# Kernel optimization log

Measured on AMD Instinct MI355X. Metric: run time of the kernel, lower is better.

The kernel has to match this reference:

```python
import jax, jax.numpy as jnp
import numpy as np

S, B, H, NL = 2048, 32, 1024, 2


def setup_inputs() -> dict:
    key = jax.random.key(0)
    k1, k2, k3, k4, k5 = jax.random.split(key, 5)
    hidden = jax.random.normal(k1, (NL, B, H), dtype=jnp.float32)
    encoder_outputs = jax.random.normal(k2, (S, B, H), dtype=jnp.float32)
    # nn.Linear(2H, H): weight [H, 2H], bias [H]
    attn_w = jax.random.normal(k3, (H, 2 * H), dtype=jnp.float32) / np.sqrt(2.0 * H)
    attn_b = jax.random.normal(k4, (H,), dtype=jnp.float32) * 0.01
    # v ~ N(0, 1/sqrt(H))
    v = jax.random.normal(k5, (H,), dtype=jnp.float32) / np.sqrt(H)
    return {"hidden": hidden, "encoder_outputs": encoder_outputs,
            "attn_w": attn_w, "attn_b": attn_b, "v": v}


def reference(hidden, encoder_outputs, attn_w, attn_b, v):
    # hidden: [NL, B, H]; encoder_outputs: [S, B, H]
    max_len = encoder_outputs.shape[0]
    h = jnp.broadcast_to(hidden[-1], (max_len,) + hidden[-1].shape)  # [S, B, H]
    x = jnp.concatenate([h, encoder_outputs], axis=2)                 # [S, B, 2H]
    energy = jnp.tanh(jnp.einsum('sbk,hk->sbh', x, attn_w) + attn_b)  # [S, B, H]
    scores = jnp.einsum('sbh,h->bs', energy, v)                       # [B, S]
    return jax.nn.softmax(scores, axis=1)
```

## Files before the change

### kernel.cpp

```cpp
#include <hip/hip_runtime.h>
#include <stdint.h>


#define S_LEN 2048
#define B_SZ 32
#define H_SZ 1024
#define M_TOT (S_LEN * B_SZ)
#define K_TOT H_SZ
#define NCB 8

typedef __attribute__((ext_vector_type(8))) short short8;
typedef __attribute__((ext_vector_type(4))) float f32x4;

static __device__ __forceinline__ unsigned short f2bf(float x) {
  uint32_t u = __builtin_bit_cast(uint32_t, x);
  u += 0x7FFFu + ((u >> 16) & 1u);
  return (unsigned short)(u >> 16);
}

static __device__ __forceinline__ float fast_tanh(float x) {
  float e = __expf(2.0f * x);
  return 1.0f - 2.0f / (e + 1.0f);
}

__global__ void __launch_bounds__(256) prep_u_kernel(
    const float* __restrict__ hidden, const float* __restrict__ attn_w,
    const float* __restrict__ attn_b, float* __restrict__ u) {
  __shared__ float hs[H_SZ];
  const int b = blockIdx.y, hc = blockIdx.x, tid = threadIdx.x;
  const float* hid = hidden + (size_t)1 * B_SZ * H_SZ + (size_t)b * H_SZ;
  for (int i = tid; i < H_SZ; i += 256) hs[i] = hid[i];
  __syncthreads();
  const int h = hc * 256 + tid;
  const float* wrow = attn_w + (size_t)h * (2 * H_SZ);
  float s = 0.f;
#pragma unroll 4
  for (int k = 0; k < H_SZ; k += 4) {
    float4 w4 = *reinterpret_cast<const float4*>(wrow + k);
    s += w4.x * hs[k] + w4.y * hs[k + 1] + w4.z * hs[k + 2] + w4.w * hs[k + 3];
  }
  u[(size_t)b * H_SZ + h] = s + attn_b[h];
}

__global__ void __launch_bounds__(256) prep_w2_kernel(
    const float* __restrict__ attn_w, unsigned short* __restrict__ Bt) {
  const int idx = blockIdx.x * 256 + threadIdx.x;
  const int base = idx * 4;
  const int n = base >> 10, k = base & 1023;
  float4 w = *reinterpret_cast<const float4*>(attn_w + (size_t)n * 2048 + 1024 + k);
  ushort4 o;
  o.x = f2bf(w.x); o.y = f2bf(w.y); o.z = f2bf(w.z); o.w = f2bf(w.w);
  *reinterpret_cast<ushort4*>(Bt + base) = o;
}

__global__ void __launch_bounds__(256) gemm_fused_kernel(
    const float* __restrict__ A,
    const unsigned short* __restrict__ Bt,
    const float* __restrict__ u,
    const float* __restrict__ v,
    float* __restrict__ pscore) {
  __shared__ unsigned short As[128 * 32];
  __shared__ unsigned short Bs[128 * 32];
  __shared__ float rowsum[2][128];

  const int tid = threadIdx.x;
  const int wid = tid >> 6, lane = tid & 63;
  const int wr = wid >> 1, wc = wid & 1;
  const int cb = blockIdx.x;
  const int brow = blockIdx.y * 128;
  const int bcol = cb * 128;

  const int arow_st = tid >> 1;
  const int acol_st = (tid & 1) * 16;
  const float* Ag = A + (size_t)(brow + arow_st) * K_TOT + acol_st;
  unsigned short* AsW = As + arow_st * 32 + acol_st;

  const int chunk0 = wid * 2;
  const unsigned short* Bg0 =
      Bt + (size_t)(bcol + chunk0 * 16 + (lane >> 2)) * K_TOT + (lane & 3) * 8;

  f32x4 acc[4][4];
#pragma unroll
  for (int i = 0; i < 4; ++i)
#pragma unroll
    for (int j = 0; j < 4; ++j) acc[i][j] = (f32x4){0.f, 0.f, 0.f, 0.f};

  const int fr = lane & 15;
  const int kseg = (lane >> 4) * 8;

  for (int k0 = 0; k0 < K_TOT; k0 += 32) {
    __syncthreads();
    const float4* ap = reinterpret_cast<const float4*>(Ag + k0);
    float4 f0 = ap[0], f1 = ap[1], f2 = ap[2], f3 = ap[3];
    uint4 w0, w1;
    w0.x = (uint32_t)f2bf(f0.x) | ((uint32_t)f2bf(f0.y) << 16);
    w0.y = (uint32_t)f2bf(f0.z) | ((uint32_t)f2bf(f0.w) << 16);
    w0.z = (uint32_t)f2bf(f1.x) | ((uint32_t)f2bf(f1.y) << 16);
    w0.w = (uint32_t)f2bf(f1.z) | ((uint32_t)f2bf(f1.w) << 16);
    w1.x = (uint32_t)f2bf(f2.x) | ((uint32_t)f2bf(f2.y) << 16);
    w1.y = (uint32_t)f2bf(f2.z) | ((uint32_t)f2bf(f2.w) << 16);
    w1.z = (uint32_t)f2bf(f3.x) | ((uint32_t)f2bf(f3.y) << 16);
    w1.w = (uint32_t)f2bf(f3.z) | ((uint32_t)f2bf(f3.w) << 16);
    *reinterpret_cast<uint4*>(AsW) = w0;
    *reinterpret_cast<uint4*>(AsW + 8) = w1;
    __builtin_amdgcn_global_load_lds(
        (const __attribute__((address_space(1))) void*)(Bg0 + k0),
        (__attribute__((address_space(3))) void*)(Bs + chunk0 * 512), 16, 0, 0);
    __builtin_amdgcn_global_load_lds(
        (const __attribute__((address_space(1))) void*)(Bg0 + 16 * K_TOT + k0),
        (__attribute__((address_space(3))) void*)(Bs + chunk0 * 512 + 512), 16, 0, 0);
    __syncthreads();

    short8 af[4], bf[4];
#pragma unroll
    for (int i = 0; i < 4; ++i)
      af[i] = *reinterpret_cast<const short8*>(As + (wr * 64 + i * 16 + fr) * 32 + kseg);
#pragma unroll
    for (int j = 0; j < 4; ++j)
      bf[j] = *reinterpret_cast<const short8*>(Bs + (wc * 64 + j * 16 + fr) * 32 + kseg);
#pragma unroll
    for (int i = 0; i < 4; ++i)
#pragma unroll
      for (int j = 0; j < 4; ++j)
        acc[i][j] = __builtin_amdgcn_mfma_f32_16x16x32_bf16(af[i], bf[j], acc[i][j], 0, 0, 0);
  }

  float vv[4];
#pragma unroll
  for (int j = 0; j < 4; ++j) vv[j] = v[bcol + wc * 64 + j * 16 + fr];

  const int g4 = (lane >> 4) * 4;
#pragma unroll
  for (int i = 0; i < 4; ++i) {
#pragma unroll
    for (int reg = 0; reg < 4; ++reg) {
      const int rloc = wr * 64 + i * 16 + g4 + reg;
      const int bb = (brow + rloc) & (B_SZ - 1);
      float rs = 0.f;
#pragma unroll
      for (int j = 0; j < 4; ++j) {
        const int h = bcol + wc * 64 + j * 16 + fr;
        float val = acc[i][j][reg] + u[(size_t)bb * H_SZ + h];
        rs += vv[j] * fast_tanh(val);
      }
      rs += __shfl_xor(rs, 1);
      rs += __shfl_xor(rs, 2);
      rs += __shfl_xor(rs, 4);
      rs += __shfl_xor(rs, 8);
      if (fr == 0) rowsum[wc][rloc] = rs;
    }
  }
  __syncthreads();
  if (tid < 128) {
    pscore[(size_t)cb * M_TOT + brow + tid] = rowsum[0][tid] + rowsum[1][tid];
  }
}

__global__ void __launch_bounds__(256) softmax_kernel(
    const float* __restrict__ ps, float* __restrict__ out) {
  const int b = blockIdx.x, tid = threadIdx.x;
  const int wid = tid >> 6, lane = tid & 63;
  __shared__ float sred[4];
  float vals[8];
  float mx = -1e30f;
#pragma unroll
  for (int ii = 0; ii < 8; ++ii) {
    const int s = ii * 256 + tid;
    float sum = 0.f;
#pragma unroll
    for (int cbk = 0; cbk < NCB; ++cbk) sum += ps[(size_t)cbk * M_TOT + s * B_SZ + b];
    vals[ii] = sum;
    mx = fmaxf(mx, sum);
  }
#pragma unroll
  for (int m = 1; m < 64; m <<= 1) mx = fmaxf(mx, __shfl_xor(mx, m));
  if (lane == 0) sred[wid] = mx;
  __syncthreads();
  mx = fmaxf(fmaxf(sred[0], sred[1]), fmaxf(sred[2], sred[3]));
  __syncthreads();
  float es = 0.f;
#pragma unroll
  for (int ii = 0; ii < 8; ++ii) {
    vals[ii] = __expf(vals[ii] - mx);
    es += vals[ii];
  }
#pragma unroll
  for (int m = 1; m < 64; m <<= 1) es += __shfl_xor(es, m);
  if (lane == 0) sred[wid] = es;
  __syncthreads();
  es = sred[0] + sred[1] + sred[2] + sred[3];
  const float inv = 1.0f / es;
#pragma unroll
  for (int ii = 0; ii < 8; ++ii) out[(size_t)b * S_LEN + ii * 256 + tid] = vals[ii] * inv;
}

extern "C" void kernel_launch(void* const* d_in, const int* in_sizes, int n_in,
                              void* d_out, int out_size, void* d_ws, size_t ws_size,
                              hipStream_t stream) {
  const float* hidden = (const float*)d_in[0];
  const float* enc    = (const float*)d_in[1];
  const float* attn_w = (const float*)d_in[2];
  const float* attn_b = (const float*)d_in[3];
  const float* v      = (const float*)d_in[4];
  float* out = (float*)d_out;

  char* w = (char*)d_ws;
  unsigned short* Bt = (unsigned short*)w;
  float* u  = (float*)(w + (size_t)2 * 1024 * 1024);
  float* ps = (float*)(w + (size_t)2 * 1024 * 1024 + 128 * 1024);

  prep_u_kernel<<<dim3(4, 32), 256, 0, stream>>>(hidden, attn_w, attn_b, u);
  prep_w2_kernel<<<1024, 256, 0, stream>>>(attn_w, Bt);
  gemm_fused_kernel<<<dim3(NCB, M_TOT / 128), 256, 0, stream>>>(enc, Bt, u, v, ps);
  softmax_kernel<<<B_SZ, 256, 0, stream>>>(ps, out);
}
```

Baseline: 406.1 us.

## Pre-convert encoder outputs to swizzled bf16 tile images and stream via LDS DMA

Measured after the change: 350.4 us. -13.7%, faster.

```diff
diff --git a/kernel.cpp b/kernel.cpp
--- a/kernel.cpp
+++ b/kernel.cpp
@@ -8,6 +8,8 @@
 #define M_TOT (S_LEN * B_SZ)
 #define K_TOT H_SZ
 #define NCB 8
+#define BK 64
+#define TILE_SHORTS 8192
 
 typedef __attribute__((ext_vector_type(8))) short short8;
 typedef __attribute__((ext_vector_type(4))) float f32x4;
@@ -17,7 +19,9 @@
   u += 0x7FFFu + ((u >> 16) & 1u);
   return (unsigned short)(u >> 16);
 }
-
+static __device__ __forceinline__ uint32_t pack2(float a, float b) {
+  return (uint32_t)f2bf(a) | ((uint32_t)f2bf(b) << 16);
+}
 static __device__ __forceinline__ float fast_tanh(float x) {
   float e = __expf(2.0f * x);
   return 1.0f - 2.0f / (e + 1.0f);
@@ -42,42 +46,60 @@
   u[(size_t)b * H_SZ + h] = s + attn_b[h];
 }
 
-__global__ void __launch_bounds__(256) prep_w2_kernel(
-    const float* __restrict__ attn_w, unsigned short* __restrict__ Bt) {
+__global__ void __launch_bounds__(256) prep_a_kernel(
+    const float* __restrict__ enc, unsigned short* __restrict__ Aimg) {
   const int idx = blockIdx.x * 256 + threadIdx.x;
-  const int base = idx * 4;
-  const int n = base >> 10, k = base & 1023;
-  float4 w = *reinterpret_cast<const float4*>(attn_w + (size_t)n * 2048 + 1024 + k);
-  ushort4 o;
-  o.x = f2bf(w.x); o.y = f2bf(w.y); o.z = f2bf(w.z); o.w = f2bf(w.w);
-  *reinterpret_cast<ushort4*>(Bt + base) = o;
-}
-
-__global__ void __launch_bounds__(256) gemm_fused_kernel(
-    const float* __restrict__ A,
-    const unsigned short* __restrict__ Bt,
-    const float* __restrict__ u,
-    const float* __restrict__ v,
+  const int m = idx >> 7, sl = idx & 127;
+  const int kb = sl >> 3, s8 = sl & 7;
+  const float4* src =
+      reinterpret_cast<const float4*>(enc + (size_t)m * K_TOT + kb * BK + s8 * 8);
+  float4 f0 = src[0], f1 = src[1];
+  uint4 o;
+  o.x = pack2(f0.x, f0.y); o.y = pack2(f0.z, f0.w);
+  o.z = pack2(f1.x, f1.y); o.w = pack2(f1.z, f1.w);
+  const int row = m & 127;
+  const size_t tile = (size_t)(m >> 7) * 16 + kb;
+  unsigned short* dst = Aimg + tile * TILE_SHORTS + row * 64 + ((s8 ^ (row & 7)) << 3);
+  *reinterpret_cast<uint4*>(dst) = o;
+}
+
+__global__ void __launch_bounds__(256) prep_b_kernel(
+    const float* __restrict__ attn_w, unsigned short* __restrict__ Bimg) {
+  const int idx = blockIdx.x * 256 + threadIdx.x;
+  const int n = idx >> 7, sl = idx & 127;
+  const int kb = sl >> 3, s8 = sl & 7;
+  const float4* src = reinterpret_cast<const float4*>(
+      attn_w + (size_t)n * 2048 + 1024 + kb * BK + s8 * 8);
+  float4 f0 = src[0], f1 = src[1];
+  uint4 o;
+  o.x = pack2(f0.x, f0.y); o.y = pack2(f0.z, f0.w);
+  o.z = pack2(f1.x, f1.y); o.w = pack2(f1.z, f1.w);
+  const int row = n & 127;
+  const size_t tile = (size_t)(n >> 7) * 16 + kb;
+  unsigned short* dst = Bimg + tile * TILE_SHORTS + row * 64 + ((s8 ^ (row & 7)) << 3);
+  *reinterpret_cast<uint4*>(dst) = o;
+}
+
+__global__ void __launch_bounds__(256) gemm_img_kernel(
+    const unsigned short* __restrict__ Aimg, const unsigned short* __restrict__ Bimg,
+    const float* __restrict__ u, const float* __restrict__ v,
     float* __restrict__ pscore) {
-  __shared__ unsigned short As[128 * 32];
-  __shared__ unsigned short Bs[128 * 32];
+  __shared__ unsigned short As[TILE_SHORTS];
+  __shared__ unsigned short Bs[TILE_SHORTS];
   __shared__ float rowsum[2][128];
 
   const int tid = threadIdx.x;
   const int wid = tid >> 6, lane = tid & 63;
   const int wr = wid >> 1, wc = wid & 1;
-  const int cb = blockIdx.x;
-  const int brow = blockIdx.y * 128;
-  const int bcol = cb * 128;
-
-  const int arow_st = tid >> 1;
-  const int acol_st = (tid & 1) * 16;
-  const float* Ag = A + (size_t)(brow + arow_st) * K_TOT + acol_st;
-  unsigned short* AsW = As + arow_st * 32 + acol_st;
-
-  const int chunk0 = wid * 2;
-  const unsigned short* Bg0 =
-      Bt + (size_t)(bcol + chunk0 * 16 + (lane >> 2)) * K_TOT + (lane & 3) * 8;
+
+  const int wg = blockIdx.x;
+  const int xcd = wg & 7, li = wg >> 3;
+  const int rp = xcd * 64 + (li >> 3);
+  const int cb = li & 7;
+  const int brow = rp * 128, bcol = cb * 128;
+
+  const unsigned short* Ag = Aimg + (size_t)rp * 16 * TILE_SHORTS;
+  const unsigned short* Bg = Bimg + (size_t)cb * 16 * TILE_SHORTS;
 
   f32x4 acc[4][4];
 #pragma unroll
@@ -85,51 +107,58 @@
 #pragma unroll
     for (int j = 0; j < 4; ++j) acc[i][j] = (f32x4){0.f, 0.f, 0.f, 0.f};
 
-  const int fr = lane & 15;
-  const int kseg = (lane >> 4) * 8;
-
-  for (int k0 = 0; k0 < K_TOT; k0 += 32) {
+  const int fr = lane & 15, g = lane >> 4;
+  const int soff0 = ((g) ^ (fr & 7)) << 3;
+  const int soff1 = ((4 + g) ^ (fr & 7)) << 3;
+  const int arow_base = (wr * 64 + fr) * 64;
+  const int brow_base = (wc * 64 + fr) * 64;
+  const int stg = wid * 2048;
+
+  for (int kb = 0; kb < 16; ++kb) {
     __syncthreads();
-    const float4* ap = reinterpret_cast<const float4*>(Ag + k0);
-    float4 f0 = ap[0], f1 = ap[1], f2 = ap[2], f3 = ap[3];
-    uint4 w0, w1;
-    w0.x = (uint32_t)f2bf(f0.x) | ((uint32_t)f2bf(f0.y) << 16);
-    w0.y = (uint32_t)f2bf(f0.z) | ((uint32_t)f2bf(f0.w) << 16);
-    w0.z = (uint32_t)f2bf(f1.x) | ((uint32_t)f2bf(f1.y) << 16);
-    w0.w = (uint32_t)f2bf(f1.z) | ((uint32_t)f2bf(f1.w) << 16);
-    w1.x = (uint32_t)f2bf(f2.x) | ((uint32_t)f2bf(f2.y) << 16);
-    w1.y = (uint32_t)f2bf(f2.z) | ((uint32_t)f2bf(f2.w) << 16);
-    w1.z = (uint32_t)f2bf(f3.x) | ((uint32_t)f2bf(f3.y) << 16);
-    w1.w = (uint32_t)f2bf(f3.z) | ((uint32_t)f2bf(f3.w) << 16);
-    *reinterpret_cast<uint4*>(AsW) = w0;
-    *reinterpret_cast<uint4*>(AsW + 8) = w1;
-    __builtin_amdgcn_global_load_lds(
-        (const __attribute__((address_space(1))) void*)(Bg0 + k0),
-        (__attribute__((address_space(3))) void*)(Bs + chunk0 * 512), 16, 0, 0);
-    __builtin_amdgcn_global_load_lds(
-        (const __attribute__((address_space(1))) void*)(Bg0 + 16 * K_TOT + k0),
-        (__attribute__((address_space(3))) void*)(Bs + chunk0 * 512 + 512), 16, 0, 0);
+    const unsigned short* at = Ag + kb * TILE_SHORTS + stg + lane * 8;
+    const unsigned short* bt = Bg + kb * TILE_SHORTS + stg + lane * 8;
+#pragma unroll
+    for (int j = 0; j < 4; ++j) {
+      __builtin_amdgcn_global_load_lds(
+          (const __attribute__((address_space(1))) void*)(at + j * 512),
+          (__attribute__((address_space(3))) void*)(As + stg + j * 512), 16, 0, 0);
+      __builtin_amdgcn_global_load_lds(
+          (const __attribute__((address_space(1))) void*)(bt + j * 512),
+          (__attribute__((address_space(3))) void*)(Bs + stg + j * 512), 16, 0, 0);
+    }
     __syncthreads();
 
     short8 af[4], bf[4];
 #pragma unroll
     for (int i = 0; i < 4; ++i)
-      af[i] = *reinterpret_cast<const short8*>(As + (wr * 64 + i * 16 + fr) * 32 + kseg);
+      af[i] = *reinterpret_cast<const short8*>(As + arow_base + i * 1024 + soff0);
 #pragma unroll
     for (int j = 0; j < 4; ++j)
-      bf[j] = *reinterpret_cast<const short8*>(Bs + (wc * 64 + j * 16 + fr) * 32 + kseg);
+      bf[j] = *reinterpret_cast<const short8*>(Bs + brow_base + j * 1024 + soff0);
 #pragma unroll
     for (int i = 0; i < 4; ++i)
 #pragma unroll
       for (int j = 0; j < 4; ++j)
         acc[i][j] = __builtin_amdgcn_mfma_f32_16x16x32_bf16(af[i], bf[j], acc[i][j], 0, 0, 0);
+#pragma unroll
+    for (int i = 0; i < 4; ++i)
+      af[i] = *reinterpret_cast<const short8*>(As + arow_base + i * 1024 + soff1);
+#pragma unroll
+    for (int j = 0; j < 4; ++j)
+      bf[j] = *reinterpret_cast<const short8*>(Bs + brow_base + j * 1024 + soff1);
+#pragma unroll
+    for (int i = 0; i < 4; ++i)
+#pragma unroll
+      for (int j = 0; j < 4; ++j)
+        acc[i][j] = __builtin_amdgcn_mfma_f32_16x16x32_bf16(af[i], bf[j], acc[i][j], 0, 0, 0);
   }
 
   float vv[4];
 #pragma unroll
   for (int j = 0; j < 4; ++j) vv[j] = v[bcol + wc * 64 + j * 16 + fr];
 
-  const int g4 = (lane >> 4) * 4;
+  const int g4 = g * 4;
 #pragma unroll
   for (int i = 0; i < 4; ++i) {
 #pragma unroll
@@ -151,9 +180,106 @@
     }
   }
   __syncthreads();
-  if (tid < 128) {
+  if (tid < 128)
     pscore[(size_t)cb * M_TOT + brow + tid] = rowsum[0][tid] + rowsum[1][tid];
-  }
+}
+
+__global__ void __launch_bounds__(256) prep_w2_flat_kernel(
+    const float* __restrict__ attn_w, unsigned short* __restrict__ Bt) {
+  const int idx = blockIdx.x * 256 + threadIdx.x;
+  const int base = idx * 4;
+  const int n = base >> 10, k = base & 1023;
+  float4 w = *reinterpret_cast<const float4*>(attn_w + (size_t)n * 2048 + 1024 + k);
+  ushort4 o;
+  o.x = f2bf(w.x); o.y = f2bf(w.y); o.z = f2bf(w.z); o.w = f2bf(w.w);
+  *reinterpret_cast<ushort4*>(Bt + base) = o;
+}
+
+__global__ void __launch_bounds__(256) gemm_fused_kernel(
+    const float* __restrict__ A, const unsigned short* __restrict__ Bt,
+    const float* __restrict__ u, const float* __restrict__ v,
+    float* __restrict__ pscore) {
+  __shared__ unsigned short As[128 * 32];
+  __shared__ unsigned short Bs[128 * 32];
+  __shared__ float rowsum[2][128];
+  const int tid = threadIdx.x;
+  const int wid = tid >> 6, lane = tid & 63;
+  const int wr = wid >> 1, wc = wid & 1;
+  const int cb = blockIdx.x;
+  const int brow = blockIdx.y * 128;
+  const int bcol = cb * 128;
+  const int arow_st = tid >> 1;
+  const int acol_st = (tid & 1) * 16;
+  const float* Ag = A + (size_t)(brow + arow_st) * K_TOT + acol_st;
+  unsigned short* AsW = As + arow_st * 32 + acol_st;
+  const int chunk0 = wid * 2;
+  const unsigned short* Bg0 =
+      Bt + (size_t)(bcol + chunk0 * 16 + (lane >> 2)) * K_TOT + (lane & 3) * 8;
+  f32x4 acc[4][4];
+#pragma unroll
+  for (int i = 0; i < 4; ++i)
+#pragma unroll
+    for (int j = 0; j < 4; ++j) acc[i][j] = (f32x4){0.f, 0.f, 0.f, 0.f};
+  const int fr = lane & 15;
+  const int kseg = (lane >> 4) * 8;
+  for (int k0 = 0; k0 < K_TOT; k0 += 32) {
+    __syncthreads();
+    const float4* ap = reinterpret_cast<const float4*>(Ag + k0);
+    float4 f0 = ap[0], f1 = ap[1], f2 = ap[2], f3 = ap[3];
+    uint4 w0, w1;
+    w0.x = pack2(f0.x, f0.y); w0.y = pack2(f0.z, f0.w);
+    w0.z = pack2(f1.x, f1.y); w0.w = pack2(f1.z, f1.w);
+    w1.x = pack2(f2.x, f2.y); w1.y = pack2(f2.z, f2.w);
+    w1.z = pack2(f3.x, f3.y); w1.w = pack2(f3.z, f3.w);
+    *reinterpret_cast<uint4*>(AsW) = w0;
+    *reinterpret_cast<uint4*>(AsW + 8) = w1;
+    __builtin_amdgcn_global_load_lds(
+        (const __attribute__((address_space(1))) void*)(Bg0 + k0),
+        (__attribute__((address_space(3))) void*)(Bs + chunk0 * 512), 16, 0, 0);
+    __builtin_amdgcn_global_load_lds(
+        (const __attribute__((address_space(1))) void*)(Bg0 + 16 * K_TOT + k0),
+        (__attribute__((address_space(3))) void*)(Bs + chunk0 * 512 + 512), 16, 0, 0);
+    __syncthreads();
+    short8 af[4], bf[4];
+#pragma unroll
+    for (int i = 0; i < 4; ++i)
+      af[i] = *reinterpret_cast<const short8*>(As + (wr * 64 + i * 16 + fr) * 32 + kseg);
+#pragma unroll
+    for (int j = 0; j < 4; ++j)
+      bf[j] = *reinterpret_cast<const short8*>(Bs + (wc * 64 + j * 16 + fr) * 32 + kseg);
+#pragma unroll
+    for (int i = 0; i < 4; ++i)
+#pragma unroll
+      for (int j = 0; j < 4; ++j)
+        acc[i][j] = __builtin_amdgcn_mfma_f32_16x16x32_bf16(af[i], bf[j], acc[i][j], 0, 0, 0);
+  }
+  float vv[4];
+#pragma unroll
+  for (int j = 0; j < 4; ++j) vv[j] = v[bcol + wc * 64 + j * 16 + fr];
+  const int g4 = (lane >> 4) * 4;
+#pragma unroll
+  for (int i = 0; i < 4; ++i) {
+#pragma unroll
+    for (int reg = 0; reg < 4; ++reg) {
+      const int rloc = wr * 64 + i * 16 + g4 + reg;
+      const int bb = (brow + rloc) & (B_SZ - 1);
+      float rs = 0.f;
+#pragma unroll
+      for (int j = 0; j < 4; ++j) {
+        const int h = bcol + wc * 64 + j * 16 + fr;
+        float val = acc[i][j][reg] + u[(size_t)bb * H_SZ + h];
+        rs += vv[j] * fast_tanh(val);
+      }
+      rs += __shfl_xor(rs, 1);
+      rs += __shfl_xor(rs, 2);
+      rs += __shfl_xor(rs, 4);
+      rs += __shfl_xor(rs, 8);
+      if (fr == 0) rowsum[wc][rloc] = rs;
+    }
+  }
+  __syncthreads();
+  if (tid < 128)
+    pscore[(size_t)cb * M_TOT + brow + tid] = rowsum[0][tid] + rowsum[1][tid];
 }
 
 __global__ void __launch_bounds__(256) softmax_kernel(
@@ -204,13 +330,29 @@
   const float* v      = (const float*)d_in[4];
   float* out = (float*)d_out;
 
+  const size_t A_BYTES = (size_t)M_TOT * K_TOT * 2;
+  const size_t B_BYTES = (size_t)K_TOT * K_TOT * 2;
+  const size_t U_BYTES = (size_t)B_SZ * H_SZ * 4;
+  const size_t P_BYTES = (size_t)NCB * M_TOT * 4;
   char* w = (char*)d_ws;
-  unsigned short* Bt = (unsigned short*)w;
-  float* u  = (float*)(w + (size_t)2 * 1024 * 1024);
-  float* ps = (float*)(w + (size_t)2 * 1024 * 1024 + 128 * 1024);
-
-  prep_u_kernel<<<dim3(4, 32), 256, 0, stream>>>(hidden, attn_w, attn_b, u);
-  prep_w2_kernel<<<1024, 256, 0, stream>>>(attn_w, Bt);
-  gemm_fused_kernel<<<dim3(NCB, M_TOT / 128), 256, 0, stream>>>(enc, Bt, u, v, ps);
-  softmax_kernel<<<B_SZ, 256, 0, stream>>>(ps, out);
-}
+
+  if (ws_size >= A_BYTES + B_BYTES + U_BYTES + P_BYTES) {
+    unsigned short* Aimg = (unsigned short*)w;
+    unsigned short* Bimg = (unsigned short*)(w + A_BYTES);
+    float* u  = (float*)(w + A_BYTES + B_BYTES);
+    float* ps = (float*)(w + A_BYTES + B_BYTES + U_BYTES);
+    prep_u_kernel<<<dim3(4, 32), 256, 0, stream>>>(hidden, attn_w, attn_b, u);
+    prep_b_kernel<<<512, 256, 0, stream>>>(attn_w, Bimg);
+    prep_a_kernel<<<M_TOT * 128 / 256, 256, 0, stream>>>(enc, Aimg);
+    gemm_img_kernel<<<NCB * (M_TOT / 128), 256, 0, stream>>>(Aimg, Bimg, u, v, ps);
+    softmax_kernel<<<B_SZ, 256, 0, stream>>>(ps, out);
+  } else {
+    unsigned short* Bt = (unsigned short*)w;
+    float* u  = (float*)(w + B_BYTES);
+    float* ps = (float*)(w + B_BYTES + U_BYTES);
+    prep_u_kernel<<<dim3(4, 32), 256, 0, stream>>>(hidden, attn_w, attn_b, u);
+    prep_w2_flat_kernel<<<1024, 256, 0, stream>>>(attn_w, Bt);
+    gemm_fused_kernel<<<dim3(NCB, M_TOT / 128), 256, 0, stream>>>(enc, Bt, u, v, ps);
+    softmax_kernel<<<B_SZ, 256, 0, stream>>>(ps, out);
+  }
+}
```
